# Performance work log

Hardware: AMD Instinct MI355X
Metric: run time of the kernel (lower is better)

## Reference

```python
import jax, jax.numpy as jnp
import numpy as np

B = 1024
N = 100  # graph_size
D = 128


def setup_inputs() -> dict:
    key = jax.random.key(0)
    k1, k2 = jax.random.split(key)
    x = jax.random.normal(k1, (B * N, D), dtype=jnp.float32)
    edge_index = jax.random.randint(k2, (2, B * N * (N - 1)), 0, N, dtype=jnp.int64)
    return {"x": x, "edge_index": edge_index, "graph_size": N}


def reference(x, edge_index, graph_size):
    # x: [B*N, D] -> [B, N, D]; edge_index is split but never used in the math.
    b = x.shape[0] // graph_size
    xb = x.reshape(b, graph_size, -1)
    # per-graph dot-product logits: [B, N, N]
    logits = jnp.einsum('bnd,bmd->bnm', xb, xb)
    # segment softmax with index j = column index of the flattened [N*N] logits:
    # normalizes over rows i for each column j -> softmax along axis=1.
    return jax.nn.softmax(logits, axis=1)
```

## Files before the change

### kernel.cpp

```cpp
#include <hip/hip_runtime.h>

#define NG 100
#define DD 128
#define NPAD 112
#define LSTRIDE 136

typedef __attribute__((ext_vector_type(8))) short bf16x8;
typedef __attribute__((ext_vector_type(4))) float floatx4;

__global__ __launch_bounds__(448, 7)
void dotdec_mfma(const float* __restrict__ x, float* __restrict__ out) {
    __shared__ __align__(16) char smraw[NG * NG * 4];
    unsigned short* xs = (unsigned short*)smraw;
    float*          fo = (float*)smraw;

    const int t    = threadIdx.x;
    const int lane = t & 63;
    const int wave = t >> 6;
    const int quad = lane >> 4;
    const int lr   = lane & 15;
    const size_t b = blockIdx.x;
    const float* xb = x   + b * (size_t)(NG * DD);
    float*       ob = out + b * (size_t)(NG * NG);

    if (t < 192) {
        int r = 100 + (t >> 4), c = t & 15;
        *(uint4*)&xs[r * LSTRIDE + c * 8] = make_uint4(0u, 0u, 0u, 0u);
    }
#pragma unroll
    for (int k = 0; k < 4; ++k) {
        int p = t + 448 * k;
        if (p < NG * 16) {
            int n = p >> 4, gp = p & 15;
            float4 v0 = ((const float4*)xb)[n * 32 + gp * 2];
            float4 v1 = ((const float4*)xb)[n * 32 + gp * 2 + 1];
            unsigned int u0 = (__float_as_uint(v0.x) >> 16) | (__float_as_uint(v0.y) & 0xffff0000u);
            unsigned int u1 = (__float_as_uint(v0.z) >> 16) | (__float_as_uint(v0.w) & 0xffff0000u);
            unsigned int u2 = (__float_as_uint(v1.x) >> 16) | (__float_as_uint(v1.y) & 0xffff0000u);
            unsigned int u3 = (__float_as_uint(v1.z) >> 16) | (__float_as_uint(v1.w) & 0xffff0000u);
            *(uint4*)&xs[n * LSTRIDE + gp * 8] = make_uint4(u0, u1, u2, u3);
        }
    }
    __syncthreads();

    floatx4 acc[7];
#pragma unroll
    for (int r = 0; r < 7; ++r) acc[r] = (floatx4){0.f, 0.f, 0.f, 0.f};
#pragma unroll
    for (int k = 0; k < 4; ++k) {
        const int koff = k * 32 + quad * 8;
        bf16x8 bb = *(const bf16x8*)&xs[(wave * 16 + lr) * LSTRIDE + koff];
#pragma unroll
        for (int r = 0; r < 7; ++r) {
            bf16x8 aa = *(const bf16x8*)&xs[(r * 16 + lr) * LSTRIDE + koff];
            acc[r] = __builtin_amdgcn_mfma_f32_16x16x32_bf16(aa, bb, acc[r], 0, 0, 0);
        }
    }

    floatx4 mx4 = acc[0];
#pragma unroll
    for (int r = 1; r < 7; ++r)
#pragma unroll
        for (int i = 0; i < 4; ++i) mx4[i] = fmaxf(mx4[i], acc[r][i]);
    float mx = fmaxf(fmaxf(mx4[0], mx4[1]), fmaxf(mx4[2], mx4[3]));
    mx = fmaxf(mx, __shfl_xor(mx, 16, 64));
    mx = fmaxf(mx, __shfl_xor(mx, 32, 64));

    floatx4 s4 = (floatx4){0.f, 0.f, 0.f, 0.f};
#pragma unroll
    for (int r = 0; r < 7; ++r)
#pragma unroll
        for (int i = 0; i < 4; ++i) {
            float e = __expf(acc[r][i] - mx);
            acc[r][i] = e;
            s4[i] += e;
        }
    float s = (s4[0] + s4[1]) + (s4[2] + s4[3]);
    s += __shfl_xor(s, 16, 64);
    s += __shfl_xor(s, 32, 64);
    const float inv = __builtin_amdgcn_rcpf(s);

    __syncthreads();

    const int m = wave * 16 + lr;
    if (m < NG) {
#pragma unroll
        for (int r = 0; r < 7; ++r)
#pragma unroll
            for (int i = 0; i < 4; ++i) {
                int n = r * 16 + quad * 4 + i;
                if (n < NG) fo[n * NG + m] = acc[r][i] * inv;
            }
    }
    __syncthreads();

#pragma unroll
    for (int k = 0; k < 6; ++k) {
        int f = t + 448 * k;
        if (f < (NG * NG) / 4)
            ((float4*)ob)[f] = *(const float4*)&fo[f * 4];
    }
}

extern "C" void kernel_launch(void* const* d_in, const int* in_sizes, int n_in,
                              void* d_out, int out_size, void* d_ws, size_t ws_size,
                              hipStream_t stream) {
    const float* x = (const float*)d_in[0];
    float* out = (float*)d_out;
    const int B = in_sizes[0] / (NG * DD);
    hipLaunchKernelGGL(dotdec_mfma, dim3(B), dim3(448), 0, stream, x, out);
}
```

Before: 158.0 us.

## Process two graphs per block with register prefetch and direct output stores

Each block now handles two graphs. The second graph's input is loaded into registers while the first graph's MFMA and softmax run, which overlaps global loads with compute. The MFMA operand roles are swapped so each lane holds four consecutive output columns, and results are written straight to global memory as float4 instead of being transposed through shared memory. Occupancy drops to 4 blocks per CU (two LDS buffers plus prefetch registers), the grid is halved, and the reductions now need 4-stage shuffles per component.

```diff
diff --git a/kernel.cpp b/kernel.cpp
--- a/kernel.cpp
+++ b/kernel.cpp
@@ -8,98 +8,137 @@
 typedef __attribute__((ext_vector_type(8))) short bf16x8;
 typedef __attribute__((ext_vector_type(4))) float floatx4;
 
-__global__ __launch_bounds__(448, 7)
-void dotdec_mfma(const float* __restrict__ x, float* __restrict__ out) {
-    __shared__ __align__(16) char smraw[NG * NG * 4];
-    unsigned short* xs = (unsigned short*)smraw;
-    float*          fo = (float*)smraw;
+__device__ __forceinline__ uint4 cvt4(float4 v0, float4 v1) {
+    unsigned int u0 = (__float_as_uint(v0.x) >> 16) | (__float_as_uint(v0.y) & 0xffff0000u);
+    unsigned int u1 = (__float_as_uint(v0.z) >> 16) | (__float_as_uint(v0.w) & 0xffff0000u);
+    unsigned int u2 = (__float_as_uint(v1.x) >> 16) | (__float_as_uint(v1.y) & 0xffff0000u);
+    unsigned int u3 = (__float_as_uint(v1.z) >> 16) | (__float_as_uint(v1.w) & 0xffff0000u);
+    return make_uint4(u0, u1, u2, u3);
+}
 
-    const int t    = threadIdx.x;
-    const int lane = t & 63;
-    const int wave = t >> 6;
-    const int quad = lane >> 4;
-    const int lr   = lane & 15;
-    const size_t b = blockIdx.x;
-    const float* xb = x   + b * (size_t)(NG * DD);
-    float*       ob = out + b * (size_t)(NG * NG);
-
-    if (t < 192) {
-        int r = 100 + (t >> 4), c = t & 15;
-        *(uint4*)&xs[r * LSTRIDE + c * 8] = make_uint4(0u, 0u, 0u, 0u);
-    }
-#pragma unroll
-    for (int k = 0; k < 4; ++k) {
-        int p = t + 448 * k;
-        if (p < NG * 16) {
-            int n = p >> 4, gp = p & 15;
-            float4 v0 = ((const float4*)xb)[n * 32 + gp * 2];
-            float4 v1 = ((const float4*)xb)[n * 32 + gp * 2 + 1];
-            unsigned int u0 = (__float_as_uint(v0.x) >> 16) | (__float_as_uint(v0.y) & 0xffff0000u);
-            unsigned int u1 = (__float_as_uint(v0.z) >> 16) | (__float_as_uint(v0.w) & 0xffff0000u);
-            unsigned int u2 = (__float_as_uint(v1.x) >> 16) | (__float_as_uint(v1.y) & 0xffff0000u);
-            unsigned int u3 = (__float_as_uint(v1.z) >> 16) | (__float_as_uint(v1.w) & 0xffff0000u);
-            *(uint4*)&xs[n * LSTRIDE + gp * 8] = make_uint4(u0, u1, u2, u3);
-        }
-    }
-    __syncthreads();
-
+__device__ __forceinline__ void compute_store(const unsigned short* xs, float* __restrict__ ob,
+                                              int wave, int quad, int lr) {
     floatx4 acc[7];
 #pragma unroll
     for (int r = 0; r < 7; ++r) acc[r] = (floatx4){0.f, 0.f, 0.f, 0.f};
 #pragma unroll
     for (int k = 0; k < 4; ++k) {
         const int koff = k * 32 + quad * 8;
-        bf16x8 bb = *(const bf16x8*)&xs[(wave * 16 + lr) * LSTRIDE + koff];
+        bf16x8 a = *(const bf16x8*)&xs[(wave * 16 + lr) * LSTRIDE + koff];
 #pragma unroll
         for (int r = 0; r < 7; ++r) {
-            bf16x8 aa = *(const bf16x8*)&xs[(r * 16 + lr) * LSTRIDE + koff];
-            acc[r] = __builtin_amdgcn_mfma_f32_16x16x32_bf16(aa, bb, acc[r], 0, 0, 0);
+            bf16x8 bb = *(const bf16x8*)&xs[(r * 16 + lr) * LSTRIDE + koff];
+            acc[r] = __builtin_amdgcn_mfma_f32_16x16x32_bf16(a, bb, acc[r], 0, 0, 0);
         }
     }
 
-    floatx4 mx4 = acc[0];
+    floatx4 mx = acc[0];
 #pragma unroll
     for (int r = 1; r < 7; ++r)
 #pragma unroll
-        for (int i = 0; i < 4; ++i) mx4[i] = fmaxf(mx4[i], acc[r][i]);
-    float mx = fmaxf(fmaxf(mx4[0], mx4[1]), fmaxf(mx4[2], mx4[3]));
-    mx = fmaxf(mx, __shfl_xor(mx, 16, 64));
-    mx = fmaxf(mx, __shfl_xor(mx, 32, 64));
+        for (int i = 0; i < 4; ++i) mx[i] = fmaxf(mx[i], acc[r][i]);
+#pragma unroll
+    for (int i = 0; i < 4; ++i) {
+        mx[i] = fmaxf(mx[i], __shfl_xor(mx[i], 1, 64));
+        mx[i] = fmaxf(mx[i], __shfl_xor(mx[i], 2, 64));
+        mx[i] = fmaxf(mx[i], __shfl_xor(mx[i], 4, 64));
+        mx[i] = fmaxf(mx[i], __shfl_xor(mx[i], 8, 64));
+    }
 
-    floatx4 s4 = (floatx4){0.f, 0.f, 0.f, 0.f};
+    floatx4 s = (floatx4){0.f, 0.f, 0.f, 0.f};
 #pragma unroll
     for (int r = 0; r < 7; ++r)
 #pragma unroll
         for (int i = 0; i < 4; ++i) {
-            float e = __expf(acc[r][i] - mx);
+            float e = __expf(acc[r][i] - mx[i]);
             acc[r][i] = e;
-            s4[i] += e;
+            s[i] += e;
         }
-    float s = (s4[0] + s4[1]) + (s4[2] + s4[3]);
-    s += __shfl_xor(s, 16, 64);
-    s += __shfl_xor(s, 32, 64);
-    const float inv = __builtin_amdgcn_rcpf(s);
+    floatx4 inv;
+#pragma unroll
+    for (int i = 0; i < 4; ++i) {
+        s[i] += __shfl_xor(s[i], 1, 64);
+        s[i] += __shfl_xor(s[i], 2, 64);
+        s[i] += __shfl_xor(s[i], 4, 64);
+        s[i] += __shfl_xor(s[i], 8, 64);
+        inv[i] = __builtin_amdgcn_rcpf(s[i]);
+    }
 
-    __syncthreads();
+    const int m0 = wave * 16 + quad * 4;
+    if (m0 < NG) {
+#pragma unroll
+        for (int r = 0; r < 7; ++r) {
+            int n = r * 16 + lr;
+            if (n < NG)
+                *(floatx4*)&ob[n * NG + m0] = acc[r] * inv;
+        }
+    }
+}
 
-    const int m = wave * 16 + lr;
-    if (m < NG) {
+__global__ __launch_bounds__(448, 4)
+void dotdec_pipe(const float* __restrict__ x, float* __restrict__ out, int nb) {
+    __shared__ unsigned short xs0[NPAD * LSTRIDE];
+    __shared__ unsigned short xs1[NPAD * LSTRIDE];
+    const int t    = threadIdx.x;
+    const int lane = t & 63;
+    const int wave = t >> 6;
+    const int quad = lane >> 4;
+    const int lr   = lane & 15;
+    const size_t g0 = 2 * (size_t)blockIdx.x;
+    const size_t g1 = g0 + 1;
+    const bool  has1 = (g1 < (size_t)nb);
+    const float* xa = x + g0 * (size_t)(NG * DD);
+    const float* xc = x + (has1 ? g1 : g0) * (size_t)(NG * DD);
+    float* oa = out + g0 * (size_t)(NG * NG);
+    float* oc = out + (has1 ? g1 : g0) * (size_t)(NG * NG);
+
+    if (t < 192) {
+        int r = 100 + (t >> 4), c = t & 15;
+        *(uint4*)&xs0[r * LSTRIDE + c * 8] = make_uint4(0u, 0u, 0u, 0u);
+    } else if (t < 384) {
+        int tt = t - 192;
+        int r = 100 + (tt >> 4), c = tt & 15;
+        *(uint4*)&xs1[r * LSTRIDE + c * 8] = make_uint4(0u, 0u, 0u, 0u);
+    }
+
 #pragma unroll
-        for (int r = 0; r < 7; ++r)
-#pragma unroll
-            for (int i = 0; i < 4; ++i) {
-                int n = r * 16 + quad * 4 + i;
-                if (n < NG) fo[n * NG + m] = acc[r][i] * inv;
-            }
+    for (int k = 0; k < 4; ++k) {
+        int p = t + 448 * k;
+        if (p < NG * 16) {
+            int n = p >> 4, gp = p & 15;
+            float4 v0 = ((const float4*)xa)[n * 32 + gp * 2];
+            float4 v1 = ((const float4*)xa)[n * 32 + gp * 2 + 1];
+            *(uint4*)&xs0[n * LSTRIDE + gp * 8] = cvt4(v0, v1);
+        }
     }
     __syncthreads();
 
+    float4 q0[4], q1[4];
+    const int np = (t < 256) ? 4 : 3;
 #pragma unroll
-    for (int k = 0; k < 6; ++k) {
-        int f = t + 448 * k;
-        if (f < (NG * NG) / 4)
-            ((float4*)ob)[f] = *(const float4*)&fo[f * 4];
+    for (int k = 0; k < 4; ++k) {
+        if (k < np) {
+            int p = t + 448 * k;
+            int n = p >> 4, gp = p & 15;
+            q0[k] = ((const float4*)xc)[n * 32 + gp * 2];
+            q1[k] = ((const float4*)xc)[n * 32 + gp * 2 + 1];
+        }
     }
+
+    compute_store(xs0, oa, wave, quad, lr);
+
+#pragma unroll
+    for (int k = 0; k < 4; ++k) {
+        if (k < np) {
+            int p = t + 448 * k;
+            int n = p >> 4, gp = p & 15;
+            *(uint4*)&xs1[n * LSTRIDE + gp * 8] = cvt4(q0[k], q1[k]);
+        }
+    }
+    __syncthreads();
+
+    if (has1)
+        compute_store(xs1, oc, wave, quad, lr);
 }
 
 extern "C" void kernel_launch(void* const* d_in, const int* in_sizes, int n_in,
@@ -108,5 +147,6 @@
     const float* x = (const float*)d_in[0];
     float* out = (float*)d_out;
     const int B = in_sizes[0] / (NG * DD);
-    hipLaunchKernelGGL(dotdec_mfma, dim3(B), dim3(448), 0, stream, x, out);
+    const int grid = (B + 1) / 2;
+    hipLaunchKernelGGL(dotdec_pipe, dim3(grid), dim3(448), 0, stream, x, out, B);
 }
```

Measured after the change: 160.6 us. No clear change (+1.7%).
